# Kernel tuning notes

Measured on AMD Instinct MI355X. Metric: run time of the kernel, lower is better.

Reference implementation:

```python
import jax, jax.numpy as jnp
import numpy as np

N = 100000
E = 1600000
IN_DIM = 128
HID = 128
OUT = 64
BN_EPS = 1e-5


def setup_inputs() -> dict:
    key = jax.random.key(0)
    ks = jax.random.split(key, 12)
    x = jax.random.normal(ks[0], (N, IN_DIM), dtype=jnp.float32)
    src = jax.random.randint(ks[1], (E,), 0, N, dtype=jnp.int64)
    dst = jax.random.randint(ks[2], (E,), 0, N, dtype=jnp.int64)
    edge_index = jnp.stack([src, dst], axis=0)
    def glorot(k, fan_in, fan_out):
        s = jnp.sqrt(6.0 / (fan_in + fan_out)).astype(jnp.float32)
        return jax.random.uniform(k, (fan_in, fan_out), jnp.float32, -s, s)
    return {
        "x": x,
        "edge_index": edge_index,
        "W1": glorot(ks[3], IN_DIM, HID), "b1": jnp.zeros((HID,), jnp.float32),
        "g1": jnp.ones((HID,), jnp.float32), "be1": jnp.zeros((HID,), jnp.float32),
        "W2": glorot(ks[4], HID, HID), "b2": jnp.zeros((HID,), jnp.float32),
        "g2": jnp.ones((HID,), jnp.float32), "be2": jnp.zeros((HID,), jnp.float32),
        "W3": glorot(ks[5], HID, OUT), "b3": jnp.zeros((OUT,), jnp.float32),
    }


def _gcn_norm(edge_index, n):
    # PyG GCNConv: add self-loops, symmetric normalization D^-1/2 (A+I) D^-1/2
    loop = jnp.arange(n, dtype=edge_index.dtype)
    src = jnp.concatenate([edge_index[0], loop])
    dst = jnp.concatenate([edge_index[1], loop])
    deg = jax.ops.segment_sum(jnp.ones_like(src, dtype=jnp.float32), dst, num_segments=n)
    dinv = jnp.where(deg > 0, jax.lax.rsqrt(deg), 0.0)
    norm = dinv[src] * dinv[dst]  # [E+N]
    return src, dst, norm


def _gcn(x, src, dst, norm, W, b, n):
    xw = x @ W                                  # [N, out]
    msg = xw[src] * norm[:, None]               # gather over edges
    return jax.ops.segment_sum(msg, dst, num_segments=n) + b


def _bn(x, g, be):
    # training-mode BatchNorm1d over node dim, biased variance
    mu = jnp.mean(x, axis=0)
    var = jnp.mean(jnp.square(x - mu), axis=0)
    return (x - mu) * jax.lax.rsqrt(var + BN_EPS) * g + be


def reference(x, edge_index, W1, b1, g1, be1, W2, b2, g2, be2, W3, b3):
    n = x.shape[0]
    src, dst, norm = _gcn_norm(edge_index, n)
    h = _gcn(x, src, dst, norm, W1, b1, n)
    h = jax.nn.relu(_bn(h, g1, be1))  # dropout = identity (eval)
    h = _gcn(h, src, dst, norm, W2, b2, n)
    h = jax.nn.relu(_bn(h, g2, be2))
    return _gcn(h, src, dst, norm, W3, b3, n)
```

## Files before the change

### kernel.cpp

```cpp
#include <hip/hip_runtime.h>
#include <cstdint>
#include <cstddef>

#define BN_EPS 1e-5f
#define BKT 256
#define BSH 9
#define CHUNK 8192

typedef __attribute__((ext_vector_type(8))) short bf16x8;
typedef __attribute__((ext_vector_type(4))) float f32x4;

__device__ __forceinline__ unsigned int f32_to_bf16_rne(float f) {
    unsigned int u = __float_as_uint(f);
    u += 0x7FFFu + ((u >> 16) & 1u);
    return u >> 16;
}
__device__ __forceinline__ unsigned int pack_bf16x2(float a, float b) {
    return f32_to_bf16_rne(a) | (f32_to_bf16_rne(b) << 16);
}
__device__ __forceinline__ float bf16_lo(unsigned int p) { return __uint_as_float(p << 16); }
__device__ __forceinline__ float bf16_hi(unsigned int p) { return __uint_as_float(p & 0xFFFF0000u); }

__global__ void hist_kernel(const int* __restrict__ dst, int* __restrict__ H, int e, int G) {
    __shared__ int h[BKT];
    int t = threadIdx.x, g = blockIdx.x;
    h[t] = 0;
    __syncthreads();
    int base = g * CHUNK;
#pragma unroll
    for (int i = 0; i < CHUNK / 256; i++) {
        int idx = base + i * 256 + t;
        if (idx < e) atomicAdd(&h[dst[idx] >> BSH], 1);
    }
    __syncthreads();
    H[t * G + g] = h[t];
}

__global__ void bin_scatter_kernel(const int* __restrict__ src, const int* __restrict__ dst,
                                   const int* __restrict__ Hscan, uint2* __restrict__ binned,
                                   int e, int G) {
    __shared__ int cur[BKT];
    int t = threadIdx.x, g = blockIdx.x;
    cur[t] = Hscan[t * G + g];
    __syncthreads();
    int base = g * CHUNK;
#pragma unroll
    for (int i = 0; i < CHUNK / 256; i++) {
        int idx = base + i * 256 + t;
        if (idx < e) {
            int s = src[idx], d = dst[idx];
            int pos = atomicAdd(&cur[d >> BSH], 1);
            uint2 v; v.x = (unsigned)s; v.y = (unsigned)d;
            binned[pos] = v;
        }
    }
}

__global__ __launch_bounds__(256) void bucket_build_kernel(const uint2* __restrict__ binned,
                                                           const int* __restrict__ Hscan,
                                                           int* __restrict__ cnt,
                                                           int* __restrict__ rowptr,
                                                           float* __restrict__ dinv,
                                                           int* __restrict__ esrc,
                                                           int e, int G, int n) {
    __shared__ int lcnt[512], lexc[512], ssum[256];
    const int t = threadIdx.x;
    const int b = blockIdx.x;
    const int start = Hscan[b * G];
    const int end = (b == BKT - 1) ? e : Hscan[(b + 1) * G];

    lcnt[t] = 0; lcnt[t + 256] = 0;
    __syncthreads();
    for (int i = start + t; i < end; i += 256)
        atomicAdd(&lcnt[binned[i].y & 511], 1);
    __syncthreads();

    int a0 = lcnt[2 * t], a1 = lcnt[2 * t + 1];
    ssum[t] = a0 + a1;
    __syncthreads();
    for (int off = 1; off < 256; off <<= 1) {
        int v = (t >= off) ? ssum[t - off] : 0;
        __syncthreads();
        ssum[t] += v;
        __syncthreads();
    }
    int excl = (t == 0) ? 0 : ssum[t - 1];
    lexc[2 * t] = excl;
    lexc[2 * t + 1] = excl + a0;
    __syncthreads();

    int nodebase = b << BSH;
#pragma unroll
    for (int j2 = 0; j2 < 2; j2++) {
        int j = 2 * t + j2;
        int node = nodebase + j;
        if (node < n) {
            int c = lcnt[j];
            cnt[node] = c;
            rowptr[node] = start + lexc[j];
            dinv[node] = rsqrtf((float)(c + 1));
        }
    }
    __syncthreads();

    for (int i = start + t; i < end; i += 256) {
        uint2 ed = binned[i];
        int pos = start + atomicAdd(&lexc[ed.y & 511], 1);
        esrc[pos] = (int)ed.x;
    }
}


__global__ void blocksum_kernel(const int* __restrict__ in, int* __restrict__ bsum, int n) {
    int t = threadIdx.x;
    int base = blockIdx.x * 1024 + t * 4;
    int s = 0;
    if (base + 3 < n) {
        int4 v = *(const int4*)&in[base];
        s = v.x + v.y + v.z + v.w;
    } else {
        for (int j = 0; j < 4; j++) if (base + j < n) s += in[base + j];
    }
    __shared__ int ls[256];
    ls[t] = s;
    __syncthreads();
    for (int off = 128; off > 0; off >>= 1) {
        if (t < off) ls[t] += ls[t + off];
        __syncthreads();
    }
    if (t == 0) bsum[blockIdx.x] = ls[0];
}

__global__ void scan_bsum_kernel(int* __restrict__ bsum, int nb) {
    int t = threadIdx.x;
    __shared__ int ls[256];
    int v = (t < nb) ? bsum[t] : 0;
    ls[t] = v;
    __syncthreads();
    for (int off = 1; off < 256; off <<= 1) {
        int p = (t >= off) ? ls[t - off] : 0;
        __syncthreads();
        ls[t] += p;
        __syncthreads();
    }
    if (t < nb) bsum[t] = ls[t] - v;
}

__global__ void scan_write1_kernel(const int* __restrict__ in, const int* __restrict__ bsum,
                                   int* __restrict__ out, int n) {
    int t = threadIdx.x;
    int base = blockIdx.x * 1024 + t * 4;
    int v[4];
    int s = 0;
    if (base + 3 < n) {
        int4 q = *(const int4*)&in[base];
        v[0] = q.x; v[1] = q.y; v[2] = q.z; v[3] = q.w;
        s = q.x + q.y + q.z + q.w;
    } else {
        for (int j = 0; j < 4; j++) { v[j] = (base + j < n) ? in[base + j] : 0; s += v[j]; }
    }
    __shared__ int ls[256];
    ls[t] = s;
    __syncthreads();
    for (int off = 1; off < 256; off <<= 1) {
        int p = (t >= off) ? ls[t - off] : 0;
        __syncthreads();
        ls[t] += p;
        __syncthreads();
    }
    int run = bsum[blockIdx.x] + ls[t] - s;
    if (base + 3 < n) {
        int4 r; r.x = run; r.y = run + v[0]; r.z = run + v[0] + v[1]; r.w = run + v[0] + v[1] + v[2];
        *(int4*)&out[base] = r;
    } else {
        for (int j = 0; j < 4; j++) {
            if (base + j < n) out[base + j] = run;
            run += v[j];
        }
    }
}


__global__ void dhist_kernel(const int* __restrict__ cnt, int* __restrict__ dh, int n) {
    __shared__ int h[256];
    int t = threadIdx.x;
    h[t] = 0;
    __syncthreads();
    for (int i = blockIdx.x * 256 + t; i < n; i += gridDim.x * 256) {
        int d = cnt[i];
        atomicAdd(&h[d > 255 ? 255 : d], 1);
    }
    __syncthreads();
    if (h[t]) atomicAdd(&dh[t], h[t]);
}

__global__ void dscan_kernel(const int* __restrict__ dh, int* __restrict__ cursor) {
    int t = threadIdx.x;
    __shared__ int ls[256];
    int v = dh[t];
    ls[t] = v;
    __syncthreads();
    for (int off = 1; off < 256; off <<= 1) {
        int p = (t >= off) ? ls[t - off] : 0;
        __syncthreads();
        ls[t] += p;
        __syncthreads();
    }
    cursor[t] = ls[t] - v;
}

__global__ void dscatter_kernel(const int* __restrict__ cnt, const int* __restrict__ rowptr,
                                const float* __restrict__ dinv, int* __restrict__ cursor,
                                int* __restrict__ perm, int* __restrict__ rowptr_p,
                                int* __restrict__ cnt_p, float* __restrict__ dinv_p, int n) {
    __shared__ int lh[256], lbase[256];
    int t = threadIdx.x;
    lh[t] = 0;
    __syncthreads();
    int i = blockIdx.x * 256 + t;
    int d = 0, b = 0, lpos = 0;
    bool ok = i < n;
    if (ok) {
        d = cnt[i];
        b = d > 255 ? 255 : d;
        lpos = atomicAdd(&lh[b], 1);
    }
    __syncthreads();
    if (lh[t]) lbase[t] = atomicAdd(&cursor[t], lh[t]);
    __syncthreads();
    if (ok) {
        int pos = lbase[b] + lpos;
        perm[pos] = i;
        rowptr_p[pos] = rowptr[i];
        cnt_p[pos] = d;
        dinv_p[pos] = dinv[i];
    }
}


__device__ __forceinline__ void wprep_one(const float* __restrict__ W,
                                          uint4* __restrict__ whi, uint4* __restrict__ wlo,
                                          int slot, int OUTC) {
    int l  = slot & 63;
    int kc = (slot >> 6) & 3;
    int ct = slot >> 8;
    int c  = ct * 16 + (l & 15);
    int k0 = kc * 32 + (l >> 4) * 8;
    unsigned hi[4], lo[4];
#pragma unroll
    for (int jj = 0; jj < 4; jj++) {
        float v0 = W[(size_t)(k0 + 2 * jj) * OUTC + c];
        float v1 = W[(size_t)(k0 + 2 * jj + 1) * OUTC + c];
        unsigned h0 = f32_to_bf16_rne(v0), h1 = f32_to_bf16_rne(v1);
        float l0 = v0 - __uint_as_float(h0 << 16);
        float l1 = v1 - __uint_as_float(h1 << 16);
        hi[jj] = h0 | (h1 << 16);
        lo[jj] = pack_bf16x2(l0, l1);
    }
    uint4 uh; uh.x = hi[0]; uh.y = hi[1]; uh.z = hi[2]; uh.w = hi[3];
    uint4 ul; ul.x = lo[0]; ul.y = lo[1]; ul.z = lo[2]; ul.w = lo[3];
    whi[slot] = uh;
    wlo[slot] = ul;
}

__global__ void wprep_all_kernel(const float* __restrict__ W1, uint4* w1hi, uint4* w1lo,
                                 const float* __restrict__ W2, uint4* w2hi, uint4* w2lo,
                                 const float* __restrict__ W3, uint4* w3hi, uint4* w3lo) {
    int id = blockIdx.x * 256 + threadIdx.x;
    if (id < 2048)       wprep_one(W1, w1hi, w1lo, id, 128);
    else if (id < 4096)  wprep_one(W2, w2hi, w2lo, id - 2048, 128);
    else if (id < 5120)  wprep_one(W3, w3hi, w3lo, id - 4096, 64);
}


template <int OUTC, bool SLAB>
__global__ __launch_bounds__(256) void gemm_kernel(const float* __restrict__ X,
                                                   const uint4* __restrict__ whi,
                                                   const uint4* __restrict__ wlo,
                                                   const float* __restrict__ scale,
                                                   const float* __restrict__ shift,
                                                   const float* __restrict__ dinv,
                                                   unsigned int* __restrict__ Y, int n) {
    constexpr int NCT = OUTC / 16;
    constexpr int CTW = NCT / 4;
    __shared__ __align__(16) unsigned short lAhi[64 * 128];
    __shared__ __align__(16) unsigned short lAlo[64 * 128];
    __shared__ float ldv[64];
    const int t = threadIdx.x;
    const int base = blockIdx.x * 64;
    const int lane = t & 63;
    const int w = t >> 6;
    const bool bn = (scale != nullptr);

    if (t < 64) { int r = base + t; ldv[t] = (r < n) ? dinv[r] : 0.0f; }

    bf16x8 bhi[CTW][4], blo[CTW][4];
#pragma unroll
    for (int c = 0; c < CTW; c++) {
        int ct = w * CTW + c;
#pragma unroll
        for (int kc = 0; kc < 4; kc++) {
            int slot = (ct * 4 + kc) * 64 + lane;
            bhi[c][kc] = *reinterpret_cast<const bf16x8*>(whi + slot);
            blo[c][kc] = *reinterpret_cast<const bf16x8*>(wlo + slot);
        }
    }

    const int col4 = (t & 31) * 4;
    float4 sc4, sh4;
    if (bn) {
        sc4 = *(const float4*)&scale[col4];
        sh4 = *(const float4*)&shift[col4];
    }
#pragma unroll
    for (int i = 0; i < 8; i++) {
        int row = i * 8 + (t >> 5);
        int r = base + row;
        float4 xv = make_float4(0.f, 0.f, 0.f, 0.f);
        if (r < n) xv = *(const float4*)&X[(size_t)r * 128 + col4];
        if (bn) {
            xv.x = fmaxf(fmaf(xv.x, sc4.x, sh4.x), 0.0f);
            xv.y = fmaxf(fmaf(xv.y, sc4.y, sh4.y), 0.0f);
            xv.z = fmaxf(fmaf(xv.z, sc4.z, sh4.z), 0.0f);
            xv.w = fmaxf(fmaf(xv.w, sc4.w, sh4.w), 0.0f);
        }
        unsigned h0 = f32_to_bf16_rne(xv.x), h1 = f32_to_bf16_rne(xv.y);
        unsigned h2 = f32_to_bf16_rne(xv.z), h3 = f32_to_bf16_rne(xv.w);
        float l0 = xv.x - __uint_as_float(h0 << 16);
        float l1 = xv.y - __uint_as_float(h1 << 16);
        float l2 = xv.z - __uint_as_float(h2 << 16);
        float l3 = xv.w - __uint_as_float(h3 << 16);
        uint2 ph; ph.x = h0 | (h1 << 16); ph.y = h2 | (h3 << 16);
        uint2 pl; pl.x = pack_bf16x2(l0, l1); pl.y = pack_bf16x2(l2, l3);
        int off = row * 256 + ((col4 * 2) ^ ((row & 7) << 4));
        *(uint2*)((char*)lAhi + off) = ph;
        *(uint2*)((char*)lAlo + off) = pl;
    }
    __syncthreads();

    const int arow = lane & 15;
    const int kb16 = (lane >> 4) * 16;
#pragma unroll
    for (int rt = 0; rt < 4; rt++) {
        f32x4 acc[CTW];
#pragma unroll
        for (int c = 0; c < CTW; c++) acc[c] = (f32x4){0.f, 0.f, 0.f, 0.f};
        int row = rt * 16 + arow;
        int rb = row * 256;
        int sw = (row & 7) << 4;
#pragma unroll
        for (int kc = 0; kc < 4; kc++) {
            int off = rb + ((kc * 64 + kb16) ^ sw);
            bf16x8 ah = *(const bf16x8*)((const char*)lAhi + off);
            bf16x8 al = *(const bf16x8*)((const char*)lAlo + off);
#pragma unroll
            for (int c = 0; c < CTW; c++) {
                acc[c] = __builtin_amdgcn_mfma_f32_16x16x32_bf16(bhi[c][kc], ah, acc[c], 0, 0, 0);
                acc[c] = __builtin_amdgcn_mfma_f32_16x16x32_bf16(blo[c][kc], ah, acc[c], 0, 0, 0);
                acc[c] = __builtin_amdgcn_mfma_f32_16x16x32_bf16(bhi[c][kc], al, acc[c], 0, 0, 0);
            }
        }
        int r = base + row;
        if (r < n) {
            float dv = ldv[row];
#pragma unroll
            for (int c = 0; c < CTW; c++) {
                int ct = w * CTW + c;
                uint2 o;
                o.x = pack_bf16x2(acc[c][0] * dv, acc[c][1] * dv);
                o.y = pack_bf16x2(acc[c][2] * dv, acc[c][3] * dv);
                if constexpr (SLAB)
                    *(uint2*)&Y[(size_t)ct * n * 8 + (size_t)r * 8 + (lane >> 4) * 2] = o;
                else
                    *(uint2*)&Y[(size_t)r * (OUTC / 2) + ct * 8 + (lane >> 4) * 2] = o;
            }
        }
    }
}


__global__ __launch_bounds__(256) void agg128s_kernel(const unsigned int* __restrict__ xw,
                                                      const int* __restrict__ rowptr_p,
                                                      const int* __restrict__ cnt_p,
                                                      const int* __restrict__ esrc,
                                                      const float* __restrict__ dinv_p,
                                                      const int* __restrict__ perm,
                                                      const float* __restrict__ bias,
                                                      float* __restrict__ out,
                                                      float* __restrict__ bnpart, int n) {
    __shared__ float lp[64][17], lq[64][17];
    __shared__ float lr[2][16][8];

    const uint2* xw2 = (const uint2*)xw;
    const int slab = blockIdx.x & 7;
    const int grp  = blockIdx.x >> 3;
    const int t = threadIdx.x;
    const int w = t >> 6;
    const int lane = t & 63;
    const int slot = lane >> 2;
    const int sub  = lane & 3;
    const int lnode = w * 16 + slot;
    const int idx = grp * 64 + lnode;
    bool ok = idx < n;
    int ic = ok ? idx : 0;

    float di = dinv_p[ic];
    int beg = rowptr_p[ic];
    int cv  = ok ? cnt_p[ic] : 0;
    int node = perm[ic];
    int last = beg + cv - 1;
    int nb = (cv + 7) >> 3;

    const size_t sbase = (size_t)slab * n * 4;
    uint2 ap = xw2[sbase + (size_t)node * 4 + sub];
    float ax = bf16_lo(ap.x), ay = bf16_hi(ap.x);
    float az = bf16_lo(ap.y), aw = bf16_hi(ap.y);

    int s[8], sn[8];
    if (nb > 0) {
#pragma unroll
        for (int j = 0; j < 8; j++) {
            int i2 = beg + j;
            s[j] = esrc[i2 <= last ? i2 : last];
        }
    }
    for (int b = 0; b < nb; b++) {
        int ebase = beg + b * 8;
        if (b + 1 < nb) {
#pragma unroll
            for (int j = 0; j < 8; j++) {
                int i2 = ebase + 8 + j;
                sn[j] = esrc[i2 <= last ? i2 : last];
            }
        }
        uint2 v[8];
#pragma unroll
        for (int j = 0; j < 8; j++) v[j] = xw2[sbase + (size_t)s[j] * 4 + sub];
        int rem = last - ebase;
#pragma unroll
        for (int j = 0; j < 8; j++) {
            float m = (j <= rem) ? 1.0f : 0.0f;
            ax = fmaf(m, bf16_lo(v[j].x), ax);
            ay = fmaf(m, bf16_hi(v[j].x), ay);
            az = fmaf(m, bf16_lo(v[j].y), az);
            aw = fmaf(m, bf16_hi(v[j].y), aw);
        }
        if (b + 1 < nb) {
#pragma unroll
            for (int j = 0; j < 8; j++) s[j] = sn[j];
        }
    }

    float4 o = make_float4(0.f, 0.f, 0.f, 0.f);
    if (ok) {
        float4 bv = ((const float4*)bias)[slab * 4 + sub];
        o.x = fmaf(di, ax, bv.x);
        o.y = fmaf(di, ay, bv.y);
        o.z = fmaf(di, az, bv.z);
        o.w = fmaf(di, aw, bv.w);
        *(float4*)(out + (size_t)node * 128 + slab * 16 + sub * 4) = o;
    }

    int c0 = sub * 4;
    lp[lnode][c0 + 0] = o.x;  lq[lnode][c0 + 0] = o.x * o.x;
    lp[lnode][c0 + 1] = o.y;  lq[lnode][c0 + 1] = o.y * o.y;
    lp[lnode][c0 + 2] = o.z;  lq[lnode][c0 + 2] = o.z * o.z;
    lp[lnode][c0 + 3] = o.w;  lq[lnode][c0 + 3] = o.w * o.w;
    __syncthreads();
    {
        int col = t & 15;
        int which = (t >> 4) & 1;
        int chunk = t >> 5;
        float srd = 0.0f;
#pragma unroll
        for (int r = 0; r < 8; r++) {
            int rr = chunk * 8 + r;
            srd += which ? lq[rr][col] : lp[rr][col];
        }
        lr[which][col][chunk] = srd;
    }
    __syncthreads();
    if (t < 32) {
        int which = t >> 4;
        int col = t & 15;
        float srd = 0.0f;
#pragma unroll
        for (int c = 0; c < 8; c++) srd += lr[which][col][c];
        bnpart[(size_t)blockIdx.x * 32 + which * 16 + col] = srd;
    }
}


__global__ __launch_bounds__(256) void agg64_kernel(const unsigned int* __restrict__ xw,
                                                    const int* __restrict__ rowptr_p,
                                                    const int* __restrict__ cnt_p,
                                                    const int* __restrict__ esrc,
                                                    const float* __restrict__ dinv_p,
                                                    const int* __restrict__ perm,
                                                    const float* __restrict__ bias,
                                                    float* __restrict__ out, int n) {
    int wid = (blockIdx.x * 256 + threadIdx.x) >> 6;
    int lane = threadIdx.x & 63;
    int half = lane >> 5;
    int hl = lane & 31;
    int idx = wid * 2 + half;
    bool ok = idx < n;
    int ic = ok ? idx : 0;

    float di = dinv_p[ic];
    int beg = rowptr_p[ic];
    int cv  = ok ? cnt_p[ic] : 0;
    int node = perm[ic];
    int last = beg + cv - 1;
    int nb = (cv + 7) >> 3;

    unsigned int ap = xw[(size_t)node * 32 + hl];
    float ax = bf16_lo(ap), ay = bf16_hi(ap);

    int s[8], sn[8];
    if (nb > 0) {
#pragma unroll
        for (int j = 0; j < 8; j++) {
            int i2 = beg + j;
            s[j] = esrc[i2 <= last ? i2 : last];
        }
    }
    for (int b = 0; b < nb; b++) {
        int ebase = beg + b * 8;
        if (b + 1 < nb) {
#pragma unroll
            for (int j = 0; j < 8; j++) {
                int i2 = ebase + 8 + j;
                sn[j] = esrc[i2 <= last ? i2 : last];
            }
        }
        unsigned int v[8];
#pragma unroll
        for (int j = 0; j < 8; j++) v[j] = xw[(size_t)s[j] * 32 + hl];
        int rem = last - ebase;
#pragma unroll
        for (int j = 0; j < 8; j++) {
            float m = (j <= rem) ? 1.0f : 0.0f;
            ax = fmaf(m, bf16_lo(v[j]), ax);
            ay = fmaf(m, bf16_hi(v[j]), ay);
        }
        if (b + 1 < nb) {
#pragma unroll
            for (int j = 0; j < 8; j++) s[j] = sn[j];
        }
    }
    if (ok) {
        float2 bv = ((const float2*)bias)[hl];
        float2 o;
        o.x = fmaf(di, ax, bv.x);
        o.y = fmaf(di, ay, bv.y);
        ((float2*)(out + (size_t)node * 64))[hl] = o;
    }
}


__global__ void bnred_slab_kernel(const float* __restrict__ part, float* __restrict__ sums,
                                  int ngrp) {
    int t = threadIdx.x;
    int which = t >> 7;
    int c = t & 127;
    int slab = c >> 4, lcol = c & 15;
    float s = 0.0f;
    for (int k = blockIdx.x; k < ngrp; k += gridDim.x)
        s += part[(size_t)(k * 8 + slab) * 32 + which * 16 + lcol];
    atomicAdd(&sums[which * 128 + c], s);
}

__global__ void bn_finalize_kernel(const float* __restrict__ sums, const float* __restrict__ g,
                                   const float* __restrict__ be, float* __restrict__ scale,
                                   float* __restrict__ shift, int n) {
    int c = threadIdx.x;
    float inv_n = 1.0f / (float)n;
    float mean = sums[c] * inv_n;
    float var = sums[128 + c] * inv_n - mean * mean;
    float rstd = rsqrtf(var + BN_EPS);
    float sc = rstd * g[c];
    scale[c] = sc;
    shift[c] = be[c] - mean * sc;
}


extern "C" void kernel_launch(void* const* d_in, const int* in_sizes, int n_in,
                              void* d_out, int out_size, void* d_ws, size_t ws_size,
                              hipStream_t stream) {
    const float* x   = (const float*)d_in[0];
    const int*   ei  = (const int*)d_in[1];
    const float* W1  = (const float*)d_in[2];
    const float* b1  = (const float*)d_in[3];
    const float* g1  = (const float*)d_in[4];
    const float* be1 = (const float*)d_in[5];
    const float* W2  = (const float*)d_in[6];
    const float* b2  = (const float*)d_in[7];
    const float* g2  = (const float*)d_in[8];
    const float* be2 = (const float*)d_in[9];
    const float* W3  = (const float*)d_in[10];
    const float* b3  = (const float*)d_in[11];

    const int n = in_sizes[0] / 128;
    const int E = in_sizes[1] / 2;
    const int* srcv = ei;
    const int* dstv = ei + E;

    const int G = (E + CHUNK - 1) / CHUNK;
    const int HN = BKT * G;
    const int NB = (n + 511) >> 9;

    char* p = (char*)d_ws;
    auto carve = [&](size_t bytes) -> char* {
        char* q = p;
        p += (bytes + 255) & ~(size_t)255;
        return q;
    };
    int*   cnt    = (int*)carve((size_t)n * 4);
    int*   rowptr = (int*)carve((size_t)n * 4);
    float* dinv   = (float*)carve((size_t)n * 4);
    int*   esrc   = (int*)carve((size_t)E * 4);
    uint2* binned = (uint2*)carve((size_t)E * 8);
    int*   H      = (int*)carve((size_t)HN * 4);
    int*   Hscan  = (int*)carve((size_t)HN * 4);
    float* sums   = (float*)carve(512 * 4);
    float* bnsc   = (float*)carve(512 * 4);
    int*   bsum   = (int*)carve(1024 * 4);
    int*   dh     = (int*)carve(512 * 4);
    int*   perm   = (int*)carve((size_t)n * 4);
    int*   rowptr_p = (int*)carve((size_t)n * 4);
    int*   cnt_p  = (int*)carve((size_t)n * 4);
    float* dinv_p = (float*)carve((size_t)n * 4);
    uint4* w1hi   = (uint4*)carve(2048 * 16);
    uint4* w1lo   = (uint4*)carve(2048 * 16);
    uint4* w2hi   = (uint4*)carve(2048 * 16);
    uint4* w2lo   = (uint4*)carve(2048 * 16);
    uint4* w3hi   = (uint4*)carve(1024 * 16);
    uint4* w3lo   = (uint4*)carve(1024 * 16);
    unsigned int* xwb = (unsigned int*)carve((size_t)n * 128 * 2);
    float* bufB   = (float*)carve((size_t)n * 128 * 4);

    float* bnpart = (float*)binned;
    int* cursor = dh + 256;

    hipMemsetAsync(sums, 0, 512 * 4, stream);
    hipMemsetAsync(dh, 0, 512 * 4, stream);

    int sbH = (HN + 1023) / 1024;

    wprep_all_kernel<<<20, 256, 0, stream>>>(W1, w1hi, w1lo, W2, w2hi, w2lo, W3, w3hi, w3lo);

    hist_kernel<<<G, 256, 0, stream>>>(dstv, H, E, G);
    blocksum_kernel<<<sbH, 256, 0, stream>>>(H, bsum, HN);
    scan_bsum_kernel<<<1, 256, 0, stream>>>(bsum, sbH);
    scan_write1_kernel<<<sbH, 256, 0, stream>>>(H, bsum, Hscan, HN);
    bin_scatter_kernel<<<G, 256, 0, stream>>>(srcv, dstv, Hscan, binned, E, G);
    bucket_build_kernel<<<NB, 256, 0, stream>>>(binned, Hscan, cnt, rowptr, dinv, esrc, E, G, n);

    int nblk = (n + 255) / 256;
    dhist_kernel<<<128, 256, 0, stream>>>(cnt, dh, n);
    dscan_kernel<<<1, 256, 0, stream>>>(dh, cursor);
    dscatter_kernel<<<nblk, 256, 0, stream>>>(cnt, rowptr, dinv, cursor,
                                              perm, rowptr_p, cnt_p, dinv_p, n);

    int gb = (n + 63) / 64;
    int ngrp = (n + 63) / 64;
    int ab = (n + 7) / 8;

    gemm_kernel<128, true><<<gb, 256, 0, stream>>>(x, w1hi, w1lo, nullptr, nullptr, dinv, xwb, n);
    agg128s_kernel<<<ngrp * 8, 256, 0, stream>>>(xwb, rowptr_p, cnt_p, esrc, dinv_p, perm, b1, bufB, bnpart, n);
    bnred_slab_kernel<<<64, 256, 0, stream>>>(bnpart, sums, ngrp);
    bn_finalize_kernel<<<1, 128, 0, stream>>>(sums, g1, be1, bnsc, bnsc + 128, n);

    gemm_kernel<128, true><<<gb, 256, 0, stream>>>(bufB, w2hi, w2lo, bnsc, bnsc + 128, dinv, xwb, n);
    agg128s_kernel<<<ngrp * 8, 256, 0, stream>>>(xwb, rowptr_p, cnt_p, esrc, dinv_p, perm, b2, bufB, bnpart, n);
    bnred_slab_kernel<<<64, 256, 0, stream>>>(bnpart, sums + 256, ngrp);
    bn_finalize_kernel<<<1, 128, 0, stream>>>(sums + 256, g2, be2, bnsc + 256, bnsc + 384, n);

    gemm_kernel<64, false><<<gb, 256, 0, stream>>>(bufB, w3hi, w3lo, bnsc + 256, bnsc + 384, dinv, xwb, n);
    agg64_kernel<<<ab, 256, 0, stream>>>(xwb, rowptr_p, cnt_p, esrc, dinv_p, perm, b3, (float*)d_out, n);
}
```

Measured before the change: 491.1 us.

## Replace global degree sort with per-block local degree sort

Replaces the three-kernel global counting sort of nodes by degree (histogram, scan, scatter) plus a memset with a single kernel that sorts each 512-node block by degree locally. This removes two launches, the global atomics and a memset. In exchange, degree balancing only holds within each 512-node window, which may leave aggregation waves less uniform across blocks. The atomic-based position assignment also makes the within-bucket order nondeterministic.

Result: no change. 490.4 us (-0.1%).

```diff
diff --git a/kernel.cpp b/kernel.cpp
--- a/kernel.cpp
+++ b/kernel.cpp
@@ -181,59 +181,52 @@
 }
 
 
-__global__ void dhist_kernel(const int* __restrict__ cnt, int* __restrict__ dh, int n) {
-    __shared__ int h[256];
-    int t = threadIdx.x;
+__global__ __launch_bounds__(256) void bsort_kernel(const int* __restrict__ cnt,
+                                                    const int* __restrict__ rowptr,
+                                                    const float* __restrict__ dinv,
+                                                    int* __restrict__ perm,
+                                                    int* __restrict__ rowptr_p,
+                                                    int* __restrict__ cnt_p,
+                                                    float* __restrict__ dinv_p, int n) {
+    __shared__ int h[256], sc[256];
+    const int t = threadIdx.x;
+    const int base = blockIdx.x << 9;
+    const int m = min(512, n - base);
+
     h[t] = 0;
     __syncthreads();
-    for (int i = blockIdx.x * 256 + t; i < n; i += gridDim.x * 256) {
-        int d = cnt[i];
-        atomicAdd(&h[d > 255 ? 255 : d], 1);
-    }
-    __syncthreads();
-    if (h[t]) atomicAdd(&dh[t], h[t]);
-}
-
-__global__ void dscan_kernel(const int* __restrict__ dh, int* __restrict__ cursor) {
-    int t = threadIdx.x;
-    __shared__ int ls[256];
-    int v = dh[t];
-    ls[t] = v;
+    int d0 = -1, d1 = -1;
+    if (t < m)       { d0 = min(cnt[base + t], 255);       atomicAdd(&h[d0], 1); }
+    if (t + 256 < m) { d1 = min(cnt[base + t + 256], 255); atomicAdd(&h[d1], 1); }
+    __syncthreads();
+
+    int v = h[t];
+    sc[t] = v;
     __syncthreads();
     for (int off = 1; off < 256; off <<= 1) {
-        int p = (t >= off) ? ls[t - off] : 0;
-        __syncthreads();
-        ls[t] += p;
-        __syncthreads();
-    }
-    cursor[t] = ls[t] - v;
-}
-
-__global__ void dscatter_kernel(const int* __restrict__ cnt, const int* __restrict__ rowptr,
-                                const float* __restrict__ dinv, int* __restrict__ cursor,
-                                int* __restrict__ perm, int* __restrict__ rowptr_p,
-                                int* __restrict__ cnt_p, float* __restrict__ dinv_p, int n) {
-    __shared__ int lh[256], lbase[256];
-    int t = threadIdx.x;
-    lh[t] = 0;
-    __syncthreads();
-    int i = blockIdx.x * 256 + t;
-    int d = 0, b = 0, lpos = 0;
-    bool ok = i < n;
-    if (ok) {
-        d = cnt[i];
-        b = d > 255 ? 255 : d;
-        lpos = atomicAdd(&lh[b], 1);
-    }
-    __syncthreads();
-    if (lh[t]) lbase[t] = atomicAdd(&cursor[t], lh[t]);
-    __syncthreads();
-    if (ok) {
-        int pos = lbase[b] + lpos;
-        perm[pos] = i;
-        rowptr_p[pos] = rowptr[i];
-        cnt_p[pos] = d;
-        dinv_p[pos] = dinv[i];
+        int p = (t >= off) ? sc[t - off] : 0;
+        __syncthreads();
+        sc[t] += p;
+        __syncthreads();
+    }
+    sc[t] -= v;
+    __syncthreads();
+
+    if (t < m) {
+        int node = base + t;
+        int pos = base + atomicAdd(&sc[d0], 1);
+        perm[pos] = node;
+        rowptr_p[pos] = rowptr[node];
+        cnt_p[pos] = cnt[node];
+        dinv_p[pos] = dinv[node];
+    }
+    if (t + 256 < m) {
+        int node = base + t + 256;
+        int pos = base + atomicAdd(&sc[d1], 1);
+        perm[pos] = node;
+        rowptr_p[pos] = rowptr[node];
+        cnt_p[pos] = cnt[node];
+        dinv_p[pos] = dinv[node];
     }
 }
 
@@ -626,7 +619,6 @@
     float* sums   = (float*)carve(512 * 4);
     float* bnsc   = (float*)carve(512 * 4);
     int*   bsum   = (int*)carve(1024 * 4);
-    int*   dh     = (int*)carve(512 * 4);
     int*   perm   = (int*)carve((size_t)n * 4);
     int*   rowptr_p = (int*)carve((size_t)n * 4);
     int*   cnt_p  = (int*)carve((size_t)n * 4);
@@ -641,10 +633,8 @@
     float* bufB   = (float*)carve((size_t)n * 128 * 4);
 
     float* bnpart = (float*)binned;
-    int* cursor = dh + 256;
 
     hipMemsetAsync(sums, 0, 512 * 4, stream);
-    hipMemsetAsync(dh, 0, 512 * 4, stream);
 
     int sbH = (HN + 1023) / 1024;
 
@@ -657,11 +647,7 @@
     bin_scatter_kernel<<<G, 256, 0, stream>>>(srcv, dstv, Hscan, binned, E, G);
     bucket_build_kernel<<<NB, 256, 0, stream>>>(binned, Hscan, cnt, rowptr, dinv, esrc, E, G, n);
 
-    int nblk = (n + 255) / 256;
-    dhist_kernel<<<128, 256, 0, stream>>>(cnt, dh, n);
-    dscan_kernel<<<1, 256, 0, stream>>>(dh, cursor);
-    dscatter_kernel<<<nblk, 256, 0, stream>>>(cnt, rowptr, dinv, cursor,
-                                              perm, rowptr_p, cnt_p, dinv_p, n);
+    bsort_kernel<<<NB, 256, 0, stream>>>(cnt, rowptr, dinv, perm, rowptr_p, cnt_p, dinv_p, n);
 
     int gb = (n + 63) / 64;
     int ngrp = (n + 63) / 64;
```
